# Kernel tuning notes

Hardware: AMD Instinct MI355X
Metric: run time of the kernel (lower is better)

## Reference

```python
import jax, jax.numpy as jnp
import numpy as np

E = 8      # num_experts
R = 32     # LoRA rank
D = 1024   # in_features (d_model)
H = 4096   # out_features of fc1 (hidden)
B = 2
S = 2048
SCALING = 1.0 / R  # lora_alpha / rank with alpha=1


def setup_inputs() -> dict:
    key = jax.random.key(0)
    ks = jax.random.split(key, 9)
    def w(k, shape, scale=0.02):
        return jax.random.normal(k, shape, dtype=jnp.float32) * scale
    return {
        "x": jax.random.normal(ks[0], (B, S, D), dtype=jnp.float32),
        "router_w": w(ks[1], (E, D)),
        "router_b": jnp.zeros((E,), jnp.float32),
        "fc1_w": w(ks[2], (H, D)),
        "fc1_b": jnp.zeros((H,), jnp.float32),
        "fc2_w": w(ks[3], (D, H)),
        "fc2_b": jnp.zeros((D,), jnp.float32),
        "A_down": w(ks[4], (E, R, D)),
        "Ab_down": jnp.zeros((E, R), jnp.float32),
        "B_down": w(ks[5], (E, H, R)),
        "Bb_down": jnp.zeros((E, H), jnp.float32),
        "A_up": w(ks[6], (E, R, H)),
        "Ab_up": jnp.zeros((E, R), jnp.float32),
        "B_up": w(ks[7], (E, D, R)),
        "Bb_up": jnp.zeros((E, D), jnp.float32),
    }


def _moe_lora(x, mask, A, Ab, Bw, Bb):
    # x: [B,S,din]; mask: one-hot [B,S,E]; A: [E,R,din]; Bw: [E,dout,R]
    # rank-stage for all experts is cheap (R=32), select per token via one-hot
    h = jnp.einsum('bsd,erd->bser', x, A) + Ab          # [B,S,E,R]
    hsel = jnp.einsum('bser,bse->bsr', h, mask)          # [B,S,R]
    out = jnp.zeros(x.shape[:2] + (Bw.shape[1],), dtype=x.dtype)
    for e in range(E):  # fixed small expert count; avoids [B,S,E,dout] blowup
        out = out + mask[..., e:e + 1] * (hsel @ Bw[e].T + Bb[e])
    return out * SCALING


def reference(x, router_w, router_b, fc1_w, fc1_b, fc2_w, fc2_b,
              A_down, Ab_down, B_down, Bb_down,
              A_up, Ab_up, B_up, Bb_up):
    logits = x @ router_w.T + router_b                   # [B,S,E]
    routing = jax.nn.softmax(logits, axis=-1)
    index = jnp.argmax(logits, axis=-1)                  # top-1 expert [B,S]
    mask = jax.nn.one_hot(index, E, dtype=x.dtype)       # y_hard [B,S,E]
    expert_choice = mask - jax.lax.stop_gradient(routing) + routing
    # down: frozen fc1 + sparse LoRA (dropout layers in eval mode -> identity)
    down = x @ fc1_w.T + fc1_b + _moe_lora(x, mask, A_down, Ab_down, B_down, Bb_down)
    a = jax.nn.gelu(down, approximate=False)             # F.gelu exact
    up = a @ fc2_w.T + fc2_b + _moe_lora(a, mask, A_up, Ab_up, B_up, Bb_up)
    return up, routing, expert_choice
```

## Files before the change

### kernel.cpp

```cpp
#include <hip/hip_runtime.h>
#include <hip/hip_bf16.h>
#include <math.h>
#include <stdint.h>

#define E_ 8
#define R_ 32
#define D_ 1024
#define H_ 4096
#define NTOK 4096
#define M_MAX 5120
#define TILES_MAX 40
#define SCALING 0.03125f

typedef __attribute__((ext_vector_type(8))) __bf16 bf16x8;
typedef __attribute__((ext_vector_type(8))) unsigned short ushort8;
typedef __attribute__((ext_vector_type(4))) float floatx4;

__device__ __forceinline__ unsigned short f2b(float f) {
    union { float f; unsigned int i; } v; v.f = f;
    unsigned int x = v.i;
    x += 0x7fffu + ((x >> 16) & 1u);
    return (unsigned short)(x >> 16);
}
__device__ __forceinline__ float gelu_fast(float v) {
    float u = v * (0.7978845608028654f + 0.0356774080857f * v * v);
    float t = __expf(-2.f * fabsf(u));
    float th = (1.f - t) * __builtin_amdgcn_rcpf(1.f + t);
    th = (u >= 0.f) ? th : -th;
    return 0.5f * v * (1.f + th);
}

#define GLOAD_LDS16(g, l) __builtin_amdgcn_global_load_lds( \
    (const __attribute__((address_space(1))) void*)(g),     \
    (__attribute__((address_space(3))) void*)(l), 16, 0, 0)

template <int N> __device__ __forceinline__ void waitcnt_vm() {
    static_assert(N == 0 || N == 8 || N == 24, "unsupported vmcnt");
    if constexpr (N == 0)       asm volatile("s_waitcnt vmcnt(0)" ::: "memory");
    else if constexpr (N == 8)  asm volatile("s_waitcnt vmcnt(8)" ::: "memory");
    else if constexpr (N == 24) asm volatile("s_waitcnt vmcnt(24)" ::: "memory");
}

__global__ __launch_bounds__(256) void k_prep(
    const float* __restrict__ w1, const float* __restrict__ w2,
    const float* __restrict__ Ad, const float* __restrict__ Bd,
    const float* __restrict__ Au, const float* __restrict__ Bu,
    unsigned short* __restrict__ w1b, unsigned short* __restrict__ w2b,
    unsigned short* __restrict__ Adb, unsigned short* __restrict__ Bdb,
    unsigned short* __restrict__ Aub, unsigned short* __restrict__ Bub,
    const float* __restrict__ x, const float* __restrict__ rw,
    const float* __restrict__ rb,
    float* __restrict__ out, int* __restrict__ idx)
{
    if (blockIdx.x < 5376) {
        long g = ((long)blockIdx.x * 256 + threadIdx.x) * 8;
        const float* src; unsigned short* dst; long off;
        if      (g <  4194304L) { src = w1; dst = w1b; off = 0; }
        else if (g <  8388608L) { src = w2; dst = w2b; off = 4194304L; }
        else if (g <  8650752L) { src = Ad; dst = Adb; off = 8388608L; }
        else if (g <  9699328L) { src = Bd; dst = Bdb; off = 8650752L; }
        else if (g < 10747904L) { src = Au; dst = Aub; off = 9699328L; }
        else                    { src = Bu; dst = Bub; off = 10747904L; }
        long i = g - off;
        float4 a = *(const float4*)(src + i);
        float4 b = *(const float4*)(src + i + 4);
        ushort8 o;
        o[0] = f2b(a.x); o[1] = f2b(a.y); o[2] = f2b(a.z); o[3] = f2b(a.w);
        o[4] = f2b(b.x); o[5] = f2b(b.y); o[6] = f2b(b.z); o[7] = f2b(b.w);
        *(ushort8*)(dst + i) = o;
        return;
    }
    const int wave = threadIdx.x >> 6, lane = threadIdx.x & 63;
    const int t = (blockIdx.x - 5376) * 4 + wave;
    const float4* xr = (const float4*)(x + (size_t)t * D_);
    float4 xv[4];
#pragma unroll
    for (int s = 0; s < 4; ++s) xv[s] = xr[lane + 64 * s];
    float acc[E_];
#pragma unroll
    for (int e = 0; e < E_; ++e) {
        const float4* wr = (const float4*)(rw + (size_t)e * D_);
        float s = 0.f;
#pragma unroll
        for (int u = 0; u < 4; ++u) {
            float4 wv = wr[lane + 64 * u];
            s += xv[u].x * wv.x + xv[u].y * wv.y + xv[u].z * wv.z + xv[u].w * wv.w;
        }
        acc[e] = s;
    }
#pragma unroll
    for (int e = 0; e < E_; ++e) {
#pragma unroll
        for (int m = 32; m > 0; m >>= 1) acc[e] += __shfl_xor(acc[e], m, 64);
        acc[e] += rb[e];
    }
    int best = 0;
#pragma unroll
    for (int e = 1; e < E_; ++e) if (acc[e] > acc[best]) best = e;
    const float mx = acc[best];
    float pr[E_]; float se = 0.f;
#pragma unroll
    for (int e = 0; e < E_; ++e) { pr[e] = expf(acc[e] - mx); se += pr[e]; }
    const float inv = 1.f / se;
    if (lane < E_) {
        float r = pr[lane] * inv;
        out[(size_t)NTOK * D_ + (size_t)t * E_ + lane] = r;
        float maskv = (lane == best) ? 1.f : 0.f;
        out[(size_t)NTOK * D_ + (size_t)NTOK * E_ + (size_t)t * E_ + lane] = (maskv - r) + r;
    }
    if (lane == 0) idx[t] = best;
}

__global__ __launch_bounds__(256) void k_scan(
    const int* __restrict__ idx, int* __restrict__ hdr,
    int* __restrict__ tile_e, int* __restrict__ gather)
{
    __shared__ int cnt[256][E_];
    __shared__ int tot[E_], base[E_];
    const int tid = threadIdx.x;
    for (int m = tid; m < M_MAX; m += 256) gather[m] = -1;
    int c[E_];
#pragma unroll
    for (int e = 0; e < E_; ++e) c[e] = 0;
    for (int t = tid * 16; t < tid * 16 + 16; ++t) c[idx[t] & 7]++;
#pragma unroll
    for (int e = 0; e < E_; ++e) cnt[tid][e] = c[e];
    __syncthreads();
    if (tid < E_) {
        int run = 0;
        for (int i = 0; i < 256; ++i) { int v = cnt[i][tid]; cnt[i][tid] = run; run += v; }
        tot[tid] = run;
    }
    __syncthreads();
    if (tid == 0) {
        int b = 0, tp = 0;
        for (int e = 0; e < E_; ++e) {
            base[e] = b;
            int nt = (tot[e] + 127) >> 7;
            for (int k = 0; k < nt; ++k) tile_e[tp++] = e;
            b += nt << 7;
        }
        hdr[0] = b;
        hdr[1] = tp;
        for (int k = tp; k < TILES_MAX; ++k) tile_e[k] = 0;
    }
    __syncthreads();
    int p[E_];
#pragma unroll
    for (int e = 0; e < E_; ++e) p[e] = base[e] + cnt[tid][e];
    for (int t = tid * 16; t < tid * 16 + 16; ++t) { int e = idx[t] & 7; gather[p[e]++] = t; }
}

__global__ __launch_bounds__(128) void k_gather(
    const float* __restrict__ x, const int* __restrict__ gather,
    unsigned short* __restrict__ xg)
{
    const int m = blockIdx.x, tid = threadIdx.x;
    const int t = gather[m];
    ushort8* dst = (ushort8*)(xg + (size_t)m * D_);
    ushort8 o;
    if ((unsigned)t < (unsigned)NTOK) {
        const float4* src = (const float4*)(x + (size_t)t * D_);
        float4 a = src[tid * 2], b = src[tid * 2 + 1];
        o[0] = f2b(a.x); o[1] = f2b(a.y); o[2] = f2b(a.z); o[3] = f2b(a.w);
        o[4] = f2b(b.x); o[5] = f2b(b.y); o[6] = f2b(b.z); o[7] = f2b(b.w);
    } else {
        o = (ushort8)(0);
    }
    dst[tid] = o;
}

__global__ __launch_bounds__(256) void k_lora_a2(
    const unsigned short* __restrict__ A,
    const unsigned short* __restrict__ W,
    const float* __restrict__ Ab,
    const int* __restrict__ hdr, const int* __restrict__ tile_e,
    unsigned short* __restrict__ outb,
    int Ktot)
{
    const int mtile = blockIdx.y;
    int ntiles = hdr[1]; if (ntiles > TILES_MAX) ntiles = TILES_MAX;
    if (mtile >= ntiles) return;
    const int e = tile_e[mtile] & 7;
    const int m0 = mtile * 128 + blockIdx.x * 32;
    const int wave = threadIdx.x >> 6, lane = threadIdx.x & 63;
    const int q = lane >> 4, l16 = lane & 15;
    const int Ks = Ktot >> 2;
    const int kbase = wave * Ks;
    const floatx4 z4 = {0.f, 0.f, 0.f, 0.f};
    floatx4 acc[2][2] = {{z4, z4}, {z4, z4}};
    const bf16x8* A0 = (const bf16x8*)(A + (size_t)(m0 + l16) * Ktot);
    const bf16x8* A1 = (const bf16x8*)(A + (size_t)(m0 + 16 + l16) * Ktot);
    const bf16x8* W0 = (const bf16x8*)(W + ((size_t)e * 32 + l16) * Ktot);
    const bf16x8* W1 = (const bf16x8*)(W + ((size_t)e * 32 + 16 + l16) * Ktot);
    for (int k = kbase; k < kbase + Ks; k += 32) {
        int u = (k >> 3) + q;
        bf16x8 a0 = A0[u], a1 = A1[u];
        bf16x8 b0 = W0[u], b1 = W1[u];
        acc[0][0] = __builtin_amdgcn_mfma_f32_16x16x32_bf16(a0, b0, acc[0][0], 0, 0, 0);
        acc[0][1] = __builtin_amdgcn_mfma_f32_16x16x32_bf16(a0, b1, acc[0][1], 0, 0, 0);
        acc[1][0] = __builtin_amdgcn_mfma_f32_16x16x32_bf16(a1, b0, acc[1][0], 0, 0, 0);
        acc[1][1] = __builtin_amdgcn_mfma_f32_16x16x32_bf16(a1, b1, acc[1][1], 0, 0, 0);
    }
    __shared__ float red[4][32][32];
#pragma unroll
    for (int mi = 0; mi < 2; ++mi)
#pragma unroll
        for (int ni = 0; ni < 2; ++ni)
#pragma unroll
            for (int r = 0; r < 4; ++r)
                red[wave][mi * 16 + q * 4 + r][ni * 16 + l16] = acc[mi][ni][r];
    __syncthreads();
    for (int i = threadIdx.x; i < 1024; i += 256) {
        int lr = i >> 5, c = i & 31;
        float s = red[0][lr][c] + red[1][lr][c] + red[2][lr][c] + red[3][lr][c];
        outb[(size_t)(m0 + lr) * 32 + c] = f2b(SCALING * (s + Ab[e * 32 + c]));
    }
}

template <int KTOT, int BM, int NOUTC, bool IS_FC1, int NSPLIT>
__global__ __launch_bounds__(BM * 2) void k_mlp9(
    const unsigned short* __restrict__ Amat,
    const unsigned short* __restrict__ Wmat,
    const float* __restrict__ bias,
    const unsigned short* __restrict__ lora_h,
    const unsigned short* __restrict__ lora_B,
    const float* __restrict__ lora_b,
    const int* __restrict__ hdr, const int* __restrict__ tile_e,
    const int* __restrict__ gather,
    unsigned short* __restrict__ outb,
    float* __restrict__ outf,
    float* __restrict__ P)
{
    constexpr int T     = BM * 2;
    constexpr int NX    = NOUTC / 256;
    constexpr int RING  = (BM == 256) ? 4 : 6;
    constexpr int NH    = (KTOT / NSPLIT) / 32;
    constexpr int LA    = (BM * 4) / T;
    constexpr int LB    = 1024 / T;
    constexpr int LTOT  = LA + LB;
    constexpr int VMST  = (RING - 2) * LTOT;
    constexpr int ASLOT = BM * 32;
    constexpr int BSLOT = 256 * 32;

    __shared__ unsigned short As[RING * ASLOT];
    __shared__ unsigned short Bs[RING * BSLOT];

    int nt = hdr[1]; if (nt > TILES_MAX) nt = TILES_MAX;
    const int ny = (BM == 256) ? ((nt + 1) >> 1) : nt;
    const int nact = NX * ny;
    const int lid = blockIdx.x + NX * blockIdx.y;
    if (lid >= nact) return;
    const int xc = lid & 7, jb = lid >> 3;
    const int qd = nact >> 3, rmn = nact & 7;
    const int tlin = xc * qd + (xc < rmn ? xc : rmn) + jb;
    const int ty = tlin / NX, tx = tlin - ty * NX;
    const int m0 = ty * BM, h0 = tx * 256;
    const int kstart = (int)blockIdx.z * (KTOT / NSPLIT);

    const int tid  = threadIdx.x;
    const int wave = tid >> 6, lane = tid & 63;
    const int l16 = lane & 15, q = lane >> 4;
    const int wm = (BM == 256) ? (wave & 1) : 0;
    const int wn = (BM == 256) ? (wave >> 1) : wave;

    const unsigned short* Abase = Amat + (size_t)m0 * KTOT + kstart;
    const unsigned short* Bbase = Wmat + (size_t)h0 * KTOT + kstart;
    const unsigned short* srcA[LA];
    const unsigned short* srcB[LB];
#pragma unroll
    for (int la = 0; la < LA; ++la) {
        int ci = tid + T * la, row = ci >> 2, j = ci & 3;
        srcA[la] = Abase + (size_t)row * KTOT + ((j ^ ((row >> 2) & 3)) << 3);
    }
#pragma unroll
    for (int lb = 0; lb < LB; ++lb) {
        int ci = tid + T * lb, row = ci >> 2, j = ci & 3;
        srcB[lb] = Bbase + (size_t)row * KTOT + ((j ^ ((row >> 2) & 3)) << 3);
    }
    auto stage = [&](int s) {
#pragma unroll
        for (int la = 0; la < LA; ++la) {
            GLOAD_LDS16(srcA[la], As + s * ASLOT + (wave * 64 + T * la) * 8);
            srcA[la] += 32;
        }
#pragma unroll
        for (int lb = 0; lb < LB; ++lb) {
            GLOAD_LDS16(srcB[lb], Bs + s * BSLOT + (wave * 64 + T * lb) * 8);
            srcB[lb] += 32;
        }
    };

    int aoff[8], boff[4];
#pragma unroll
    for (int mi = 0; mi < 8; ++mi) {
        int row = wm * 128 + mi * 16 + l16;
        aoff[mi] = row * 32 + ((q ^ ((row >> 2) & 3)) << 3);
    }
#pragma unroll
    for (int ni = 0; ni < 4; ++ni) {
        int row = wn * 64 + ni * 16 + l16;
        boff[ni] = row * 32 + ((q ^ ((row >> 2) & 3)) << 3);
    }

    const floatx4 z4 = {0.f, 0.f, 0.f, 0.f};
    floatx4 acc[8][4];
#pragma unroll
    for (int mi = 0; mi < 8; ++mi)
#pragma unroll
        for (int ni = 0; ni < 4; ++ni) acc[mi][ni] = z4;

#pragma unroll
    for (int h = 0; h < RING - 1; ++h) stage(h);
    waitcnt_vm<VMST>();
    __builtin_amdgcn_s_barrier();

    int slot = 0, sstage = RING - 1;
#pragma unroll 1
    for (int h = 0; h < NH; ++h) {
        bf16x8 af[8], bfr[4];
        const unsigned short* Abuf = As + slot * ASLOT;
        const unsigned short* Bbuf = Bs + slot * BSLOT;
#pragma unroll
        for (int mi = 0; mi < 8; ++mi) af[mi]  = *(const bf16x8*)(Abuf + aoff[mi]);
#pragma unroll
        for (int ni = 0; ni < 4; ++ni) bfr[ni] = *(const bf16x8*)(Bbuf + boff[ni]);
        const bool more = h < NH - (RING - 1);
        if (more) stage(sstage);
        __builtin_amdgcn_s_setprio(1);
#pragma unroll
        for (int mi = 0; mi < 8; ++mi)
#pragma unroll
            for (int ni = 0; ni < 4; ++ni)
                acc[mi][ni] = __builtin_amdgcn_mfma_f32_16x16x32_bf16(af[mi], bfr[ni], acc[mi][ni], 0, 0, 0);
        __builtin_amdgcn_s_setprio(0);
        if (more) waitcnt_vm<VMST>();
        else      waitcnt_vm<0>();
        __builtin_amdgcn_s_barrier();
        slot   = (slot   + 1 == RING) ? 0 : slot   + 1;
        sstage = (sstage + 1 == RING) ? 0 : sstage + 1;
    }

    const bool extras = (NSPLIT == 1) || (blockIdx.z == 0);
    const int e = tile_e[ty * (BM / 128) + wm] & 7;
    if (extras) {
        bf16x8 a2[8], b2[4];
#pragma unroll
        for (int mi = 0; mi < 8; ++mi)
            a2[mi] = *(const bf16x8*)(lora_h + (size_t)(m0 + wm * 128 + mi * 16 + l16) * 32 + q * 8);
#pragma unroll
        for (int ni = 0; ni < 4; ++ni)
            b2[ni] = *(const bf16x8*)(lora_B + ((size_t)e * NOUTC + h0 + wn * 64 + ni * 16 + l16) * 32 + q * 8);
#pragma unroll
        for (int mi = 0; mi < 8; ++mi)
#pragma unroll
            for (int ni = 0; ni < 4; ++ni)
                acc[mi][ni] = __builtin_amdgcn_mfma_f32_16x16x32_bf16(a2[mi], b2[ni], acc[mi][ni], 0, 0, 0);
    }

#pragma unroll
    for (int ni = 0; ni < 4; ++ni) {
        const int gh = h0 + wn * 64 + ni * 16 + l16;
        const float bv = extras ? (bias[gh] + SCALING * lora_b[e * NOUTC + gh]) : 0.f;
#pragma unroll
        for (int mi = 0; mi < 8; ++mi) {
            const int gmb = m0 + wm * 128 + mi * 16 + q * 4;
#pragma unroll
            for (int r = 0; r < 4; ++r) {
                const int gm = gmb + r;
                const float v = acc[mi][ni][r] + bv;
                if (IS_FC1) {
                    outb[(size_t)gm * NOUTC + gh] = f2b(gelu_fast(v));
                } else if (extras) {
                    const int t = gather[gm];
                    if ((unsigned)t < (unsigned)NTOK) outf[(size_t)t * NOUTC + gh] = v;
                } else {
                    P[(size_t)gm * NOUTC + gh] = v;
                }
            }
        }
    }
}

__global__ __launch_bounds__(256) void k_reduce(
    const float* __restrict__ P, const int* __restrict__ gather,
    float* __restrict__ out)
{
    const int m = blockIdx.x;
    const int t = gather[m];
    if ((unsigned)t >= (unsigned)NTOK) return;
    const float4* p4 = (const float4*)(P + (size_t)m * D_);
    float4* o4 = (float4*)(out + (size_t)t * D_);
    int i = threadIdx.x;
    float4 a = o4[i], b = p4[i];
    a.x += b.x; a.y += b.y; a.z += b.z; a.w += b.w;
    o4[i] = a;
}

#define OFF_IDX      0u
#define OFF_HDR      16384u
#define OFF_TILE     16640u
#define OFF_GATHER   16896u
#define OFF_XG       37376u
#define OFF_W1B      10523136u
#define OFF_ADB      18911744u
#define OFF_BDB      19436032u
#define OFF_HSB      21533184u
#define OFF_P        37376u
#define OFF_AG       21860864u
#define OFF_HUB      63803904u
#define OFF_W2B      64131584u
#define OFF_AUB      72520192u
#define OFF_BUB      74617344u
#define WS_NEEDED    75141632u

extern "C" void kernel_launch(void* const* d_in, const int* in_sizes, int n_in,
                              void* d_out, int out_size, void* d_ws, size_t ws_size,
                              hipStream_t stream)
{
    (void)out_size;
    if (ws_size < (size_t)WS_NEEDED) return;
    if (n_in < 15 || in_sizes[0] != NTOK * D_ || in_sizes[3] != H_ * D_ ||
        in_sizes[5] != D_ * H_ || in_sizes[9] != E_ * H_ * R_) return;

    const float* x   = (const float*)d_in[0];
    const float* rw  = (const float*)d_in[1];
    const float* rb  = (const float*)d_in[2];
    const float* w1  = (const float*)d_in[3];
    const float* b1  = (const float*)d_in[4];
    const float* w2  = (const float*)d_in[5];
    const float* b2  = (const float*)d_in[6];
    const float* Ad  = (const float*)d_in[7];
    const float* Abd = (const float*)d_in[8];
    const float* Bd  = (const float*)d_in[9];
    const float* Bbd = (const float*)d_in[10];
    const float* Au  = (const float*)d_in[11];
    const float* Abu = (const float*)d_in[12];
    const float* Bu  = (const float*)d_in[13];
    const float* Bbu = (const float*)d_in[14];
    float* out = (float*)d_out;
    char* ws = (char*)d_ws;

    int* idx            = (int*)(ws + OFF_IDX);
    int* hdr            = (int*)(ws + OFF_HDR);
    int* tile_e         = (int*)(ws + OFF_TILE);
    int* gather         = (int*)(ws + OFF_GATHER);
    unsigned short* xg  = (unsigned short*)(ws + OFF_XG);
    unsigned short* hsb = (unsigned short*)(ws + OFF_HSB);
    unsigned short* ag  = (unsigned short*)(ws + OFF_AG);
    unsigned short* hub = (unsigned short*)(ws + OFF_HUB);
    unsigned short* w1b = (unsigned short*)(ws + OFF_W1B);
    unsigned short* w2b = (unsigned short*)(ws + OFF_W2B);
    unsigned short* Adb = (unsigned short*)(ws + OFF_ADB);
    unsigned short* Bdb = (unsigned short*)(ws + OFF_BDB);
    unsigned short* Aub = (unsigned short*)(ws + OFF_AUB);
    unsigned short* Bub = (unsigned short*)(ws + OFF_BUB);
    float* P            = (float*)(ws + OFF_P);

    k_prep<<<6400, 256, 0, stream>>>(w1, w2, Ad, Bd, Au, Bu,
                                     w1b, w2b, Adb, Bdb, Aub, Bub,
                                     x, rw, rb, out, idx);
    k_scan<<<1, 256, 0, stream>>>(idx, hdr, tile_e, gather);
    k_gather<<<M_MAX, 128, 0, stream>>>(x, gather, xg);
    k_lora_a2<<<dim3(4, TILES_MAX), 256, 0, stream>>>(xg, Adb, Abd, hdr, tile_e, hsb, D_);
    k_mlp9<D_, 256, H_, true, 1><<<dim3(16, 20, 1), 512, 0, stream>>>(
        xg, w1b, b1, hsb, Bdb, Bbd, hdr, tile_e, gather, ag, nullptr, nullptr);
    k_lora_a2<<<dim3(4, TILES_MAX), 256, 0, stream>>>(ag, Aub, Abu, hdr, tile_e, hub, H_);
    k_mlp9<H_, 128, D_, false, 2><<<dim3(4, 40, 2), 256, 0, stream>>>(
        ag, w2b, b2, hub, Bub, Bbu, hdr, tile_e, gather, nullptr, out, P);
    k_reduce<<<M_MAX, 256, 0, stream>>>(P, gather, out);
}
```

Measured before the change: 339.6 us.

## Unify MLP GEMM kernel on 256x256 tiles with new LDS swizzle

```diff
diff --git a/kernel.cpp b/kernel.cpp
--- a/kernel.cpp
+++ b/kernel.cpp
@@ -35,10 +35,9 @@
     (__attribute__((address_space(3))) void*)(l), 16, 0, 0)
 
 template <int N> __device__ __forceinline__ void waitcnt_vm() {
-    static_assert(N == 0 || N == 8 || N == 24, "unsupported vmcnt");
-    if constexpr (N == 0)       asm volatile("s_waitcnt vmcnt(0)" ::: "memory");
-    else if constexpr (N == 8)  asm volatile("s_waitcnt vmcnt(8)" ::: "memory");
-    else if constexpr (N == 24) asm volatile("s_waitcnt vmcnt(24)" ::: "memory");
+    static_assert(N == 0 || N == 8, "unsupported vmcnt");
+    if constexpr (N == 0) asm volatile("s_waitcnt vmcnt(0)" ::: "memory");
+    else                  asm volatile("s_waitcnt vmcnt(8)" ::: "memory");
 }
 
 __global__ __launch_bounds__(256) void k_prep(
@@ -218,8 +217,8 @@
     }
 }
 
-template <int KTOT, int BM, int NOUTC, bool IS_FC1, int NSPLIT>
-__global__ __launch_bounds__(BM * 2) void k_mlp9(
+template <int KTOT, bool IS_FC1, int NSPLIT>
+__global__ __launch_bounds__(512) void k_mlp9(
     const unsigned short* __restrict__ Amat,
     const unsigned short* __restrict__ Wmat,
     const float* __restrict__ bias,
@@ -230,77 +229,73 @@
     const int* __restrict__ gather,
     unsigned short* __restrict__ outb,
     float* __restrict__ outf,
-    float* __restrict__ P)
-{
-    constexpr int T     = BM * 2;
-    constexpr int NX    = NOUTC / 256;
-    constexpr int RING  = (BM == 256) ? 4 : 6;
+    float* __restrict__ P,
+    int NOUTC)
+{
+    constexpr int RING  = 4;
     constexpr int NH    = (KTOT / NSPLIT) / 32;
-    constexpr int LA    = (BM * 4) / T;
-    constexpr int LB    = 1024 / T;
-    constexpr int LTOT  = LA + LB;
-    constexpr int VMST  = (RING - 2) * LTOT;
-    constexpr int ASLOT = BM * 32;
+    constexpr int ASLOT = 256 * 32;
     constexpr int BSLOT = 256 * 32;
 
     __shared__ unsigned short As[RING * ASLOT];
     __shared__ unsigned short Bs[RING * BSLOT];
 
+    const int NX = NOUTC / 256;
     int nt = hdr[1]; if (nt > TILES_MAX) nt = TILES_MAX;
-    const int ny = (BM == 256) ? ((nt + 1) >> 1) : nt;
+    const int ny = (nt + 1) >> 1;
     const int nact = NX * ny;
     const int lid = blockIdx.x + NX * blockIdx.y;
     if (lid >= nact) return;
     const int xc = lid & 7, jb = lid >> 3;
     const int qd = nact >> 3, rmn = nact & 7;
     const int tlin = xc * qd + (xc < rmn ? xc : rmn) + jb;
-    const int ty = tlin / NX, tx = tlin - ty * NX;
-    const int m0 = ty * BM, h0 = tx * 256;
+    const int ty = tlin % ny, tx = tlin / ny;
+    const int m0 = ty * 256, h0 = tx * 256;
     const int kstart = (int)blockIdx.z * (KTOT / NSPLIT);
 
     const int tid  = threadIdx.x;
     const int wave = tid >> 6, lane = tid & 63;
     const int l16 = lane & 15, q = lane >> 4;
-    const int wm = (BM == 256) ? (wave & 1) : 0;
-    const int wn = (BM == 256) ? (wave >> 1) : wave;
+    const int wm = wave & 1, wn = wave >> 1;
 
     const unsigned short* Abase = Amat + (size_t)m0 * KTOT + kstart;
     const unsigned short* Bbase = Wmat + (size_t)h0 * KTOT + kstart;
-    const unsigned short* srcA[LA];
-    const unsigned short* srcB[LB];
-#pragma unroll
-    for (int la = 0; la < LA; ++la) {
-        int ci = tid + T * la, row = ci >> 2, j = ci & 3;
-        srcA[la] = Abase + (size_t)row * KTOT + ((j ^ ((row >> 2) & 3)) << 3);
-    }
-#pragma unroll
-    for (int lb = 0; lb < LB; ++lb) {
-        int ci = tid + T * lb, row = ci >> 2, j = ci & 3;
-        srcB[lb] = Bbase + (size_t)row * KTOT + ((j ^ ((row >> 2) & 3)) << 3);
+    const unsigned short* srcA[2];
+    const unsigned short* srcB[2];
+#pragma unroll
+    for (int l = 0; l < 2; ++l) {
+        int o = tid + 512 * l;
+        int row2 = o >> 3, cp = o & 7;
+        int c = cp ^ (row2 & 7);
+        int row = 2 * row2 + (c >> 2), kch = c & 3;
+        srcA[l] = Abase + (size_t)row * KTOT + kch * 8;
+        srcB[l] = Bbase + (size_t)row * KTOT + kch * 8;
     }
     auto stage = [&](int s) {
 #pragma unroll
-        for (int la = 0; la < LA; ++la) {
-            GLOAD_LDS16(srcA[la], As + s * ASLOT + (wave * 64 + T * la) * 8);
-            srcA[la] += 32;
+        for (int l = 0; l < 2; ++l) {
+            GLOAD_LDS16(srcA[l], As + s * ASLOT + (wave * 64 + 512 * l) * 8);
+            srcA[l] += 32;
         }
 #pragma unroll
-        for (int lb = 0; lb < LB; ++lb) {
-            GLOAD_LDS16(srcB[lb], Bs + s * BSLOT + (wave * 64 + T * lb) * 8);
-            srcB[lb] += 32;
+        for (int l = 0; l < 2; ++l) {
+            GLOAD_LDS16(srcB[l], Bs + s * BSLOT + (wave * 64 + 512 * l) * 8);
+            srcB[l] += 32;
         }
     };
 
     int aoff[8], boff[4];
 #pragma unroll
     for (int mi = 0; mi < 8; ++mi) {
-        int row = wm * 128 + mi * 16 + l16;
-        aoff[mi] = row * 32 + ((q ^ ((row >> 2) & 3)) << 3);
+        int ar = wm * 128 + mi * 16 + l16;
+        int off16 = (ar >> 1) * 8 + ((((ar & 1) * 4 + q)) ^ ((ar >> 1) & 7));
+        aoff[mi] = off16 * 8;
     }
 #pragma unroll
     for (int ni = 0; ni < 4; ++ni) {
-        int row = wn * 64 + ni * 16 + l16;
-        boff[ni] = row * 32 + ((q ^ ((row >> 2) & 3)) << 3);
+        int br = wn * 64 + ni * 16 + l16;
+        int off16 = (br >> 1) * 8 + ((((br & 1) * 4 + q)) ^ ((br >> 1) & 7));
+        boff[ni] = off16 * 8;
     }
 
     const floatx4 z4 = {0.f, 0.f, 0.f, 0.f};
@@ -310,9 +305,8 @@
 #pragma unroll
         for (int ni = 0; ni < 4; ++ni) acc[mi][ni] = z4;
 
-#pragma unroll
-    for (int h = 0; h < RING - 1; ++h) stage(h);
-    waitcnt_vm<VMST>();
+    stage(0); stage(1); stage(2);
+    waitcnt_vm<8>();
     __builtin_amdgcn_s_barrier();
 
     int slot = 0, sstage = RING - 1;
@@ -334,7 +328,7 @@
             for (int ni = 0; ni < 4; ++ni)
                 acc[mi][ni] = __builtin_amdgcn_mfma_f32_16x16x32_bf16(af[mi], bfr[ni], acc[mi][ni], 0, 0, 0);
         __builtin_amdgcn_s_setprio(0);
-        if (more) waitcnt_vm<VMST>();
+        if (more) waitcnt_vm<8>();
         else      waitcnt_vm<0>();
         __builtin_amdgcn_s_barrier();
         slot   = (slot   + 1 == RING) ? 0 : slot   + 1;
@@ -342,7 +336,7 @@
     }
 
     const bool extras = (NSPLIT == 1) || (blockIdx.z == 0);
-    const int e = tile_e[ty * (BM / 128) + wm] & 7;
+    const int e = tile_e[ty * 2 + wm] & 7;
     if (extras) {
         bf16x8 a2[8], b2[4];
 #pragma unroll
@@ -463,10 +457,10 @@
     k_scan<<<1, 256, 0, stream>>>(idx, hdr, tile_e, gather);
     k_gather<<<M_MAX, 128, 0, stream>>>(x, gather, xg);
     k_lora_a2<<<dim3(4, TILES_MAX), 256, 0, stream>>>(xg, Adb, Abd, hdr, tile_e, hsb, D_);
-    k_mlp9<D_, 256, H_, true, 1><<<dim3(16, 20, 1), 512, 0, stream>>>(
-        xg, w1b, b1, hsb, Bdb, Bbd, hdr, tile_e, gather, ag, nullptr, nullptr);
+    k_mlp9<D_, true, 1><<<dim3(16, 20, 1), 512, 0, stream>>>(
+        xg, w1b, b1, hsb, Bdb, Bbd, hdr, tile_e, gather, ag, nullptr, nullptr, H_);
     k_lora_a2<<<dim3(4, TILES_MAX), 256, 0, stream>>>(ag, Aub, Abu, hdr, tile_e, hub, H_);
-    k_mlp9<H_, 128, D_, false, 2><<<dim3(4, 40, 2), 256, 0, stream>>>(
-        ag, w2b, b2, hub, Bub, Bbu, hdr, tile_e, gather, nullptr, out, P);
+    k_mlp9<H_, false, 2><<<dim3(4, 20, 2), 512, 0, stream>>>(
+        ag, w2b, b2, hub, Bub, Bbu, hdr, tile_e, gather, nullptr, out, P, D_);
     k_reduce<<<M_MAX, 256, 0, stream>>>(P, gather, out);
 }
```

New measurement: 329.3 us. 3.0% less time.
